# Optimization experiments

Hardware: AMD Instinct MI355X
Metric: run time of the kernel (lower is better)

Reference implementation:

```python
import jax, jax.numpy as jnp
import numpy as np

DIM = 512
NUM_HEADS = 8
BALL_SIZE = 64
TOPK = 2
DIMENSIONALITY = 3
B = 2
N_BALLS = 1024
N_TOTAL = B * N_BALLS * BALL_SIZE


def setup_inputs() -> dict:
    key = jax.random.key(0)
    ks = jax.random.split(key, 6)
    s = 0.02
    return {
        "x": jax.random.normal(ks[0], (N_TOTAL, DIM), jnp.float32),
        "pos": jax.random.normal(ks[1], (N_TOTAL, DIMENSIONALITY), jnp.float32),
        "qkv_w": jax.random.normal(ks[2], (DIM, 3 * DIM), jnp.float32) * s,
        "qkv_b": jnp.zeros((3 * DIM,), jnp.float32),
        "proj_w": jax.random.normal(ks[3], (DIM, DIM), jnp.float32) * s,
        "proj_b": jnp.zeros((DIM,), jnp.float32),
        "pe_w": jax.random.normal(ks[4], (DIMENSIONALITY, DIM), jnp.float32) * s,
        "pe_b": jnp.zeros((DIM,), jnp.float32),
        "num_batches": B,
    }


def _forward(x, pos, qkv_w, qkv_b, proj_w, proj_b, pe_w, pe_b, num_batches):
    N, D = x.shape
    m = BALL_SIZE
    H = NUM_HEADS
    E = D // H
    b = num_batches
    n = N // (b * m)

    # relative position of leaves wrt ball center (torch.no_grad in original)
    p = pos.reshape(-1, m, pos.shape[-1])
    rel = (p - p.mean(axis=1, keepdims=True)).reshape(N, -1)
    rel = jax.lax.stop_gradient(rel)
    x = x + rel @ pe_w + pe_b

    # qkv split exactly like repeat('(b n m) (H E K) -> K b H n m E'): K innermost
    qkv = (x @ qkv_w + qkv_b).reshape(b, n, m, H, E, 3)
    q = jnp.transpose(qkv[..., 0], (0, 3, 1, 2, 4))  # [b,H,n,m,E]
    k = jnp.transpose(qkv[..., 1], (0, 3, 1, 2, 4))
    v = jnp.transpose(qkv[..., 2], (0, 3, 1, 2, 4))

    # The original's rearrange('b n H m E -> b H n m E') on an already
    # [b,H,n,m,E] tensor swaps head/ball axes; the subsequent repeat along a
    # fresh axis of size m*E followed by gather(dim=2) picks values that are
    # independent of the topk indices. Net effect (exactly reproduced here):
    #   desired_{k,v}[b, h, query, t, m2, e] = {k,v}[b, head=t, ball=h, m2, e]
    # i.e. every query of head h attends to keys/values of ball h taken from
    # the first `topk` heads, flattened in (t, m2) order.
    k_sel = jnp.transpose(k[:, :TOPK, :H], (0, 2, 1, 3, 4)).reshape(b, H, TOPK * m, E)
    v_sel = jnp.transpose(v[:, :TOPK, :H], (0, 2, 1, 3, 4)).reshape(b, H, TOPK * m, E)

    qf = q.reshape(b, H, n * m, E)
    scores = jnp.einsum('bhqe,bhke->bhqk', qf, k_sel) * (E ** -0.5)
    attn = jax.nn.softmax(scores, axis=-1)
    out = jnp.einsum('bhqk,bhke->bhqe', attn, v_sel)  # [b,H,n*m,E]
    out = jnp.transpose(out, (0, 2, 1, 3)).reshape(N, D)  # '(b nm) (H E)'
    return out @ proj_w + proj_b


def reference(x, pos, qkv_w, qkv_b, proj_w, proj_b, pe_w, pe_b, num_batches):
    return _forward(x, pos, qkv_w, qkv_b, proj_w, proj_b, pe_w, pe_b, num_batches)
```

## Files before the change

### kernel.cpp

```cpp
#include <hip/hip_runtime.h>

typedef __bf16 bf16;
typedef __bf16 bf16x8 __attribute__((ext_vector_type(8)));
typedef __bf16 bf16x4 __attribute__((ext_vector_type(4)));
typedef float  f32x4  __attribute__((ext_vector_type(4)));

__device__ __forceinline__ f32x4 mfma16(bf16x8 a, bf16x8 b, f32x4 c) {
    return __builtin_amdgcn_mfma_f32_16x16x32_bf16(a, b, c, 0, 0, 0);
}

__device__ __forceinline__ void gll16(const bf16* g, bf16* l) {
    __builtin_amdgcn_global_load_lds(
        (const __attribute__((address_space(1))) void*)g,
        (__attribute__((address_space(3))) void*)l, 16, 0, 0);
}

__global__ __launch_bounds__(256) void prep_weights(
    const float* __restrict__ qkv_w, const float* __restrict__ qkv_b,
    const float* __restrict__ proj_w,
    bf16* __restrict__ BqT, bf16* __restrict__ kvWT, bf16* __restrict__ projWT,
    float* __restrict__ bq, float* __restrict__ bkv)
{
    int i = blockIdx.x * 256 + threadIdx.x;
    if (i < 262144) {
        int c_ = i >> 9, k = i & 511;
        int c = (c_ >> 6) * 192 + (c_ & 63) * 3;
        BqT[i] = (bf16)(qkv_w[k * 1536 + c] * 0.125f);
        return;
    }
    i -= 262144;
    if (i < 131072) {
        int c2 = i >> 9, k = i & 511;
        int t = c2 >> 7, kk = (c2 >> 6) & 1, e = c2 & 63;
        int c = t * 192 + e * 3 + 1 + kk;
        kvWT[i] = (bf16)(qkv_w[k * 1536 + c]);
        return;
    }
    i -= 131072;
    if (i < 262144) {
        int c_ = i >> 9, k = i & 511;
        projWT[i] = (bf16)(proj_w[k * 512 + c_]);
        return;
    }
    i -= 262144;
    if (i < 512) {
        bq[i] = qkv_b[(i >> 6) * 192 + (i & 63) * 3] * 0.125f;
        return;
    }
    i -= 512;
    if (i < 256) {
        int t = i >> 7, kk = (i >> 6) & 1, e = i & 63;
        bkv[i] = qkv_b[t * 192 + e * 3 + 1 + kk];
    }
}

__global__ __launch_bounds__(256) void xprep(
    const float* __restrict__ x, const float* __restrict__ pos,
    const float* __restrict__ pe_w, const float* __restrict__ pe_b,
    bf16* __restrict__ xp)
{
    const int ball = blockIdx.x;
    const int tid = threadIdx.x;
    const size_t tok0 = (size_t)ball * 64;

    __shared__ float pw[1536];
    __shared__ float pb[512];
    __shared__ float pp[64][3];
    __shared__ float mean[3];

    for (int i = tid; i < 1536; i += 256) pw[i] = pe_w[i];
    for (int i = tid; i < 512; i += 256) pb[i] = pe_b[i];
    if (tid < 64) {
        pp[tid][0] = pos[(tok0 + tid) * 3 + 0];
        pp[tid][1] = pos[(tok0 + tid) * 3 + 1];
        pp[tid][2] = pos[(tok0 + tid) * 3 + 2];
    }
    __syncthreads();
    if (tid < 3) {
        float s = 0.f;
        #pragma unroll
        for (int i = 0; i < 64; ++i) s += pp[i][tid];
        mean[tid] = s * (1.0f / 64.0f);
    }
    __syncthreads();

    const float4* x4 = (const float4*)(x + tok0 * 512);
    bf16* op = xp + tok0 * 512;
    #pragma unroll 4
    for (int it = 0; it < 32; ++it) {
        int flat = it * 256 + tid;
        int row = flat >> 7;
        int c = (flat & 127) * 4;
        float4 xv = x4[flat];
        float r0 = pp[row][0] - mean[0];
        float r1 = pp[row][1] - mean[1];
        float r2 = pp[row][2] - mean[2];
        float v0 = xv.x + r0 * pw[c + 0] + r1 * pw[512 + c + 0] + r2 * pw[1024 + c + 0] + pb[c + 0];
        float v1 = xv.y + r0 * pw[c + 1] + r1 * pw[512 + c + 1] + r2 * pw[1024 + c + 1] + pb[c + 1];
        float v2 = xv.z + r0 * pw[c + 2] + r1 * pw[512 + c + 2] + r2 * pw[1024 + c + 2] + pb[c + 2];
        float v3 = xv.w + r0 * pw[c + 3] + r1 * pw[512 + c + 3] + r2 * pw[1024 + c + 3] + pb[c + 3];
        bf16x4 ov = { (bf16)v0, (bf16)v1, (bf16)v2, (bf16)v3 };
        *(bf16x4*)(op + (size_t)flat * 4) = ov;
    }
}

template<int EPI>
__global__ __launch_bounds__(256) void gemm_bt(
    const bf16* __restrict__ A, const bf16* __restrict__ Bt,
    const float* __restrict__ bias, void* __restrict__ Cv)
{
    const int bid = blockIdx.x;
    const int ct = bid & 3;
    const int rt = bid >> 2;
    const int row0 = rt * 128, col0 = ct * 128;
    const int tid = threadIdx.x;
    const int w = tid >> 6, l = tid & 63;
    const int wr = w >> 1, wc = w & 1;
    const int l15 = l & 15, lg = l >> 4;

    __shared__ __align__(16) bf16 As[128 * 64];
    __shared__ __align__(16) bf16 Bs[128 * 64];

    f32x4 acc[4][4] = {};

    int srow[4], scol[4];
    #pragma unroll
    for (int j = 0; j < 4; ++j) {
        int chunk = w * 4 + j;
        int o = chunk * 512 + l * 8;
        int r = o >> 6;
        int slot = (o & 63) >> 3;
        srow[j] = r;
        scol[j] = ((slot ^ (r & 7)) << 3);
    }

    for (int ks = 0; ks < 512; ks += 64) {
        #pragma unroll
        for (int j = 0; j < 4; ++j) {
            int chunk = w * 4 + j;
            gll16(A  + (size_t)(row0 + srow[j]) * 512 + ks + scol[j], &As[chunk * 512]);
            gll16(Bt + (size_t)(col0 + srow[j]) * 512 + ks + scol[j], &Bs[chunk * 512]);
        }
        __syncthreads();
        #pragma unroll
        for (int kk = 0; kk < 2; ++kk) {
            bf16x8 a[4], b[4];
            #pragma unroll
            for (int mi = 0; mi < 4; ++mi) {
                int r = wr * 64 + mi * 16 + l15;
                int slot = (kk * 4 + lg) ^ (r & 7);
                a[mi] = *(const bf16x8*)&As[r * 64 + slot * 8];
            }
            #pragma unroll
            for (int ni = 0; ni < 4; ++ni) {
                int r = wc * 64 + ni * 16 + l15;
                int slot = (kk * 4 + lg) ^ (r & 7);
                b[ni] = *(const bf16x8*)&Bs[r * 64 + slot * 8];
            }
            #pragma unroll
            for (int mi = 0; mi < 4; ++mi)
                #pragma unroll
                for (int ni = 0; ni < 4; ++ni)
                    acc[mi][ni] = mfma16(a[mi], b[ni], acc[mi][ni]);
        }
        __syncthreads();
    }

    #pragma unroll
    for (int mi = 0; mi < 4; ++mi) {
        #pragma unroll
        for (int ni = 0; ni < 4; ++ni) {
            int col = col0 + wc * 64 + ni * 16 + l15;
            float bv = bias[col];
            int rbase = row0 + wr * 64 + mi * 16 + lg * 4;
            #pragma unroll
            for (int r = 0; r < 4; ++r) {
                float vv = acc[mi][ni][r] + bv;
                if (EPI == 0) ((bf16*)Cv)[(size_t)(rbase + r) * 512 + col] = (bf16)vv;
                else          ((float*)Cv)[(size_t)(rbase + r) * 512 + col] = vv;
            }
        }
    }
}

__global__ __launch_bounds__(256) void kv_proj(
    const bf16* __restrict__ xp, const bf16* __restrict__ kvWT,
    const float* __restrict__ bkv, bf16* __restrict__ ksel, bf16* __restrict__ vselT)
{
    const int bid = blockIdx.x;
    const int b = bid >> 9;
    const int ball = (bid >> 6) & 7;
    const int m2 = bid & 63;
    const size_t tok = (size_t)b * 65536 + ball * 64 + m2;
    const int tid = threadIdx.x;

    __shared__ __align__(16) bf16 xrow[512];
    xrow[tid] = xp[tok * 512 + tid];
    xrow[tid + 256] = xp[tok * 512 + tid + 256];
    __syncthreads();

    float acc = 0.f;
    const bf16* wrp = kvWT + (size_t)tid * 512;
    #pragma unroll 8
    for (int k = 0; k < 512; k += 8) {
        bf16x8 wv = *(const bf16x8*)(wrp + k);
        bf16x8 xv = *(const bf16x8*)(&xrow[k]);
        #pragma unroll
        for (int j = 0; j < 8; ++j) acc += (float)xv[j] * (float)wv[j];
    }
    acc += bkv[tid];
    int t = tid >> 7, kk = (tid >> 6) & 1, e = tid & 63;
    if (kk == 0)
        ksel[((size_t)(b * 8 + ball) * 128 + t * 64 + m2) * 64 + e] = (bf16)acc;
    else
        vselT[((size_t)(b * 8 + ball) * 64 + e) * 128 + t * 64 + m2] = (bf16)acc;
}

__global__ __launch_bounds__(256) void attn_k(
    const bf16* __restrict__ q, const bf16* __restrict__ ksel,
    const bf16* __restrict__ vselT, bf16* __restrict__ attno)
{
    const int bid = blockIdx.x;
    const int qt = bid & 1023;
    const int bh = bid >> 10;
    const int b = bh >> 3;
    const int h = bh & 7;
    const int tid = threadIdx.x;
    const int w = tid >> 6;
    const int l = tid & 63;
    const int l15 = l & 15, lg = l >> 4;

    __shared__ __align__(16) bf16 Ks[128][72];
    __shared__ __align__(16) bf16 Vt[64][136];
    __shared__ __align__(16) bf16 Pl[4][16][136];

    const bf16* kg = ksel + (size_t)(b * 8 + h) * 128 * 64;
    #pragma unroll
    for (int it = 0; it < 8; ++it) {
        int i = it * 256 + tid;
        int r = i >> 4, c4 = (i & 15) * 4;
        *(bf16x4*)&Ks[r][c4] = *(const bf16x4*)(kg + r * 64 + c4);
    }
    const bf16* vg = vselT + (size_t)(b * 8 + h) * 64 * 128;
    #pragma unroll
    for (int it = 0; it < 8; ++it) {
        int i = it * 256 + tid;
        int r = i >> 5, c4 = (i & 31) * 4;
        *(bf16x4*)&Vt[r][c4] = *(const bf16x4*)(vg + r * 128 + c4);
    }

    const size_t tokq = (size_t)b * 65536 + (size_t)qt * 64 + w * 16 + l15;
    const bf16* qp = q + tokq * 512 + h * 64 + lg * 8;
    bf16x8 qa0 = *(const bf16x8*)qp;
    bf16x8 qa1 = *(const bf16x8*)(qp + 32);

    __syncthreads();

    f32x4 s[8];
    #pragma unroll
    for (int kt = 0; kt < 8; ++kt) {
        f32x4 a0 = {0.f, 0.f, 0.f, 0.f};
        a0 = mfma16(qa0, *(const bf16x8*)&Ks[kt * 16 + l15][lg * 8], a0);
        a0 = mfma16(qa1, *(const bf16x8*)&Ks[kt * 16 + l15][32 + lg * 8], a0);
        s[kt] = a0;
    }

    #pragma unroll
    for (int r = 0; r < 4; ++r) {
        float mx = s[0][r];
        #pragma unroll
        for (int kt = 1; kt < 8; ++kt) mx = fmaxf(mx, s[kt][r]);
        mx = fmaxf(mx, __shfl_xor(mx, 1));
        mx = fmaxf(mx, __shfl_xor(mx, 2));
        mx = fmaxf(mx, __shfl_xor(mx, 4));
        mx = fmaxf(mx, __shfl_xor(mx, 8));
        float sum = 0.f;
        #pragma unroll
        for (int kt = 0; kt < 8; ++kt) {
            float p = __expf(s[kt][r] - mx);
            s[kt][r] = p;
            sum += p;
        }
        sum += __shfl_xor(sum, 1);
        sum += __shfl_xor(sum, 2);
        sum += __shfl_xor(sum, 4);
        sum += __shfl_xor(sum, 8);
        float inv = 1.0f / sum;
        int prow = lg * 4 + r;
        #pragma unroll
        for (int kt = 0; kt < 8; ++kt)
            Pl[w][prow][kt * 16 + l15] = (bf16)(s[kt][r] * inv);
    }

    __syncthreads();

    f32x4 o[4] = { {0,0,0,0}, {0,0,0,0}, {0,0,0,0}, {0,0,0,0} };
    #pragma unroll
    for (int kc = 0; kc < 4; ++kc) {
        bf16x8 pa = *(const bf16x8*)&Pl[w][l15][kc * 32 + lg * 8];
        #pragma unroll
        for (int et = 0; et < 4; ++et)
            o[et] = mfma16(pa, *(const bf16x8*)&Vt[et * 16 + l15][kc * 32 + lg * 8], o[et]);
    }

    const size_t tokw = (size_t)b * 65536 + (size_t)qt * 64 + w * 16 + lg * 4;
    #pragma unroll
    for (int et = 0; et < 4; ++et)
        #pragma unroll
        for (int r = 0; r < 4; ++r)
            attno[(tokw + r) * 512 + h * 64 + et * 16 + l15] = (bf16)(o[et][r]);
}

extern "C" void kernel_launch(void* const* d_in, const int* in_sizes, int n_in,
                              void* d_out, int out_size, void* d_ws, size_t ws_size,
                              hipStream_t stream) {
    (void)in_sizes; (void)n_in; (void)out_size; (void)ws_size;
    const float* x      = (const float*)d_in[0];
    const float* pos    = (const float*)d_in[1];
    const float* qkv_w  = (const float*)d_in[2];
    const float* qkv_b  = (const float*)d_in[3];
    const float* proj_w = (const float*)d_in[4];
    const float* proj_b = (const float*)d_in[5];
    const float* pe_w   = (const float*)d_in[6];
    const float* pe_b   = (const float*)d_in[7];

    char* ws = (char*)d_ws;
    bf16*  Z     = (bf16*)(ws);
    bf16*  Q     = (bf16*)(ws + 134217728);
    bf16*  BqT   = (bf16*)(ws + 268435456);
    bf16*  PjT   = (bf16*)(ws + 268959744);
    bf16*  kvWT  = (bf16*)(ws + 269484032);
    bf16*  ksel  = (bf16*)(ws + 269746176);
    bf16*  vselT = (bf16*)(ws + 270008320);
    float* bq    = (float*)(ws + 270270464);
    float* bkv   = (float*)(ws + 270272512);

    prep_weights<<<2563, 256, 0, stream>>>(qkv_w, qkv_b, proj_w, BqT, kvWT, PjT, bq, bkv);
    xprep<<<2048, 256, 0, stream>>>(x, pos, pe_w, pe_b, Z);
    gemm_bt<0><<<4096, 256, 0, stream>>>(Z, BqT, bq, (void*)Q);
    kv_proj<<<1024, 256, 0, stream>>>(Z, kvWT, bkv, ksel, vselT);
    attn_k<<<16384, 256, 0, stream>>>(Q, ksel, vselT, Z);
    gemm_bt<1><<<4096, 256, 0, stream>>>(Z, PjT, proj_b, d_out);
}
```

Measured before the change: 512.1 us.

## Fold positional embedding into Q GEMM and fuse attention with output projection

```diff
diff --git a/kernel.cpp b/kernel.cpp
--- a/kernel.cpp
+++ b/kernel.cpp
@@ -19,7 +19,7 @@
     const float* __restrict__ qkv_w, const float* __restrict__ qkv_b,
     const float* __restrict__ proj_w,
     bf16* __restrict__ BqT, bf16* __restrict__ kvWT, bf16* __restrict__ projWT,
-    float* __restrict__ bq, float* __restrict__ bkv)
+    float* __restrict__ bkv)
 {
     int i = blockIdx.x * 256 + threadIdx.x;
     if (i < 262144) {
@@ -43,83 +43,81 @@
         return;
     }
     i -= 262144;
-    if (i < 512) {
-        bq[i] = qkv_b[(i >> 6) * 192 + (i & 63) * 3] * 0.125f;
-        return;
-    }
-    i -= 512;
     if (i < 256) {
         int t = i >> 7, kk = (i >> 6) & 1, e = i & 63;
         bkv[i] = qkv_b[t * 192 + e * 3 + 1 + kk];
     }
 }
 
-__global__ __launch_bounds__(256) void xprep(
-    const float* __restrict__ x, const float* __restrict__ pos,
+__global__ __launch_bounds__(256) void prep_r(
+    const float* __restrict__ qkv_w, const float* __restrict__ qkv_b,
     const float* __restrict__ pe_w, const float* __restrict__ pe_b,
-    bf16* __restrict__ xp)
-{
-    const int ball = blockIdx.x;
-    const int tid = threadIdx.x;
-    const size_t tok0 = (size_t)ball * 64;
-
-    __shared__ float pw[1536];
-    __shared__ float pb[512];
-    __shared__ float pp[64][3];
-    __shared__ float mean[3];
-
-    for (int i = tid; i < 1536; i += 256) pw[i] = pe_w[i];
-    for (int i = tid; i < 512; i += 256) pb[i] = pe_b[i];
-    if (tid < 64) {
-        pp[tid][0] = pos[(tok0 + tid) * 3 + 0];
-        pp[tid][1] = pos[(tok0 + tid) * 3 + 1];
-        pp[tid][2] = pos[(tok0 + tid) * 3 + 2];
-    }
-    __syncthreads();
-    if (tid < 3) {
-        float s = 0.f;
-        #pragma unroll
-        for (int i = 0; i < 64; ++i) s += pp[i][tid];
-        mean[tid] = s * (1.0f / 64.0f);
-    }
-    __syncthreads();
-
-    const float4* x4 = (const float4*)(x + tok0 * 512);
-    bf16* op = xp + tok0 * 512;
-    #pragma unroll 4
-    for (int it = 0; it < 32; ++it) {
-        int flat = it * 256 + tid;
-        int row = flat >> 7;
-        int c = (flat & 127) * 4;
-        float4 xv = x4[flat];
-        float r0 = pp[row][0] - mean[0];
-        float r1 = pp[row][1] - mean[1];
-        float r2 = pp[row][2] - mean[2];
-        float v0 = xv.x + r0 * pw[c + 0] + r1 * pw[512 + c + 0] + r2 * pw[1024 + c + 0] + pb[c + 0];
-        float v1 = xv.y + r0 * pw[c + 1] + r1 * pw[512 + c + 1] + r2 * pw[1024 + c + 1] + pb[c + 1];
-        float v2 = xv.z + r0 * pw[c + 2] + r1 * pw[512 + c + 2] + r2 * pw[1024 + c + 2] + pb[c + 2];
-        float v3 = xv.w + r0 * pw[c + 3] + r1 * pw[512 + c + 3] + r2 * pw[1024 + c + 3] + pb[c + 3];
-        bf16x4 ov = { (bf16)v0, (bf16)v1, (bf16)v2, (bf16)v3 };
-        *(bf16x4*)(op + (size_t)flat * 4) = ov;
-    }
-}
-
-template<int EPI>
-__global__ __launch_bounds__(256) void gemm_bt(
-    const bf16* __restrict__ A, const bf16* __restrict__ Bt,
-    const float* __restrict__ bias, void* __restrict__ Cv)
-{
-    const int bid = blockIdx.x;
-    const int ct = bid & 3;
-    const int rt = bid >> 2;
+    float* __restrict__ R, float* __restrict__ bq2)
+{
+    int idx = blockIdx.x * 256 + threadIdx.x;
+    int c = idx >> 2, j = idx & 3;
+    int qc = (c >> 6) * 192 + (c & 63) * 3;
+    const float* wcol = qkv_w + qc;
+    float s = 0.f;
+    if (j < 3) {
+        const float* pw = pe_w + j * 512;
+        for (int k = 0; k < 512; ++k) s += pw[k] * wcol[(size_t)k * 1536];
+        R[j * 512 + c] = 0.125f * s;
+    } else {
+        for (int k = 0; k < 512; ++k) s += pe_b[k] * wcol[(size_t)k * 1536];
+        bq2[c] = 0.125f * (qkv_b[qc] + s);
+    }
+}
+
+__global__ __launch_bounds__(64) void relprep(const float* __restrict__ pos,
+                                              float* __restrict__ rel)
+{
+    const int t = blockIdx.x * 64 + threadIdx.x;
+    float p0 = pos[(size_t)t * 3 + 0];
+    float p1 = pos[(size_t)t * 3 + 1];
+    float p2 = pos[(size_t)t * 3 + 2];
+    float s0 = p0, s1 = p1, s2 = p2;
+    #pragma unroll
+    for (int m = 1; m < 64; m <<= 1) {
+        s0 += __shfl_xor(s0, m);
+        s1 += __shfl_xor(s1, m);
+        s2 += __shfl_xor(s2, m);
+    }
+    rel[(size_t)t * 3 + 0] = p0 - s0 * (1.0f / 64.0f);
+    rel[(size_t)t * 3 + 1] = p1 - s1 * (1.0f / 64.0f);
+    rel[(size_t)t * 3 + 2] = p2 - s2 * (1.0f / 64.0f);
+}
+
+__global__ __launch_bounds__(256, 2) void qgemm(
+    const float* __restrict__ X, const bf16* __restrict__ Bt,
+    const float* __restrict__ rel, const float* __restrict__ R,
+    const float* __restrict__ bq2, bf16* __restrict__ Qout)
+{
+    const int bid0 = blockIdx.x;
+    const int wg = (bid0 & 7) * 512 + (bid0 >> 3);
+    const int ct = wg & 3;
+    const int rt = wg >> 2;
     const int row0 = rt * 128, col0 = ct * 128;
     const int tid = threadIdx.x;
     const int w = tid >> 6, l = tid & 63;
     const int wr = w >> 1, wc = w & 1;
     const int l15 = l & 15, lg = l >> 4;
 
-    __shared__ __align__(16) bf16 As[128 * 64];
-    __shared__ __align__(16) bf16 Bs[128 * 64];
+    __shared__ __align__(16) bf16 As[8192];
+    __shared__ __align__(16) bf16 Bs[8192];
+    __shared__ float relS[128][3];
+    __shared__ float RS[3][128];
+
+    if (tid < 128) {
+        relS[tid][0] = rel[(size_t)(row0 + tid) * 3 + 0];
+        relS[tid][1] = rel[(size_t)(row0 + tid) * 3 + 1];
+        relS[tid][2] = rel[(size_t)(row0 + tid) * 3 + 2];
+    } else {
+        int c = tid - 128;
+        RS[0][c] = R[0 * 512 + col0 + c];
+        RS[1][c] = R[1 * 512 + col0 + c];
+        RS[2][c] = R[2 * 512 + col0 + c];
+    }
 
     f32x4 acc[4][4] = {};
 
@@ -133,12 +131,25 @@
         srow[j] = r;
         scol[j] = ((slot ^ (r & 7)) << 3);
     }
+    const int ar_sub = l >> 3;
+    const int ak = l & 7;
+    const int aslot = (ak ^ ar_sub) << 3;
 
     for (int ks = 0; ks < 512; ks += 64) {
         #pragma unroll
         for (int j = 0; j < 4; ++j) {
             int chunk = w * 4 + j;
-            gll16(A  + (size_t)(row0 + srow[j]) * 512 + ks + scol[j], &As[chunk * 512]);
+            int r = chunk * 8 + ar_sub;
+            const float* xp = X + (size_t)(row0 + r) * 512 + ks + ak * 8;
+            float4 v0 = *(const float4*)xp;
+            float4 v1 = *(const float4*)(xp + 4);
+            bf16x8 bv = { (bf16)v0.x, (bf16)v0.y, (bf16)v0.z, (bf16)v0.w,
+                          (bf16)v1.x, (bf16)v1.y, (bf16)v1.z, (bf16)v1.w };
+            *(bf16x8*)&As[r * 64 + aslot] = bv;
+        }
+        #pragma unroll
+        for (int j = 0; j < 4; ++j) {
+            int chunk = w * 4 + j;
             gll16(Bt + (size_t)(col0 + srow[j]) * 512 + ks + scol[j], &Bs[chunk * 512]);
         }
         __syncthreads();
@@ -170,22 +181,27 @@
     for (int mi = 0; mi < 4; ++mi) {
         #pragma unroll
         for (int ni = 0; ni < 4; ++ni) {
-            int col = col0 + wc * 64 + ni * 16 + l15;
-            float bv = bias[col];
-            int rbase = row0 + wr * 64 + mi * 16 + lg * 4;
+            int colL = wc * 64 + ni * 16 + l15;
+            int col = col0 + colL;
+            float bv = bq2[col];
+            float r0c = RS[0][colL], r1c = RS[1][colL], r2c = RS[2][colL];
+            int rbaseL = wr * 64 + mi * 16 + lg * 4;
             #pragma unroll
             for (int r = 0; r < 4; ++r) {
-                float vv = acc[mi][ni][r] + bv;
-                if (EPI == 0) ((bf16*)Cv)[(size_t)(rbase + r) * 512 + col] = (bf16)vv;
-                else          ((float*)Cv)[(size_t)(rbase + r) * 512 + col] = vv;
-            }
-        }
-    }
-}
-
-__global__ __launch_bounds__(256) void kv_proj(
-    const bf16* __restrict__ xp, const bf16* __restrict__ kvWT,
-    const float* __restrict__ bkv, bf16* __restrict__ ksel, bf16* __restrict__ vselT)
+                int rowL = rbaseL + r;
+                float vv = acc[mi][ni][r] + bv
+                         + relS[rowL][0] * r0c + relS[rowL][1] * r1c + relS[rowL][2] * r2c;
+                Qout[(size_t)(row0 + rowL) * 512 + col] = (bf16)vv;
+            }
+        }
+    }
+}
+
+__global__ __launch_bounds__(256) void kv_proj2(
+    const float* __restrict__ x, const float* __restrict__ rel,
+    const float* __restrict__ pe_w, const float* __restrict__ pe_b,
+    const bf16* __restrict__ kvWT, const float* __restrict__ bkv,
+    bf16* __restrict__ ksel, bf16* __restrict__ vselT)
 {
     const int bid = blockIdx.x;
     const int b = bid >> 9;
@@ -195,8 +211,14 @@
     const int tid = threadIdx.x;
 
     __shared__ __align__(16) bf16 xrow[512];
-    xrow[tid] = xp[tok * 512 + tid];
-    xrow[tid + 256] = xp[tok * 512 + tid + 256];
+    __shared__ float relt[3];
+    if (tid < 3) relt[tid] = rel[tok * 3 + tid];
+    __syncthreads();
+    for (int k = tid; k < 512; k += 256) {
+        float v = x[tok * 512 + k] + relt[0] * pe_w[k] + relt[1] * pe_w[512 + k]
+                + relt[2] * pe_w[1024 + k] + pe_b[k];
+        xrow[k] = (bf16)v;
+    }
     __syncthreads();
 
     float acc = 0.f;
@@ -216,99 +238,130 @@
         vselT[((size_t)(b * 8 + ball) * 64 + e) * 128 + t * 64 + m2] = (bf16)acc;
 }
 
-__global__ __launch_bounds__(256) void attn_k(
-    const bf16* __restrict__ q, const bf16* __restrict__ ksel,
-    const bf16* __restrict__ vselT, bf16* __restrict__ attno)
+__global__ __launch_bounds__(256, 2) void attnproj(
+    const bf16* __restrict__ Q, const bf16* __restrict__ ksel,
+    const bf16* __restrict__ vselT, const bf16* __restrict__ projT,
+    const float* __restrict__ proj_b, float* __restrict__ out)
 {
     const int bid = blockIdx.x;
-    const int qt = bid & 1023;
-    const int bh = bid >> 10;
-    const int b = bh >> 3;
-    const int h = bh & 7;
+    const int wg = (bid & 7) * 256 + (bid >> 3);
+    const int b = wg >> 10;
+    const size_t tok0 = (size_t)wg * 64;
     const int tid = threadIdx.x;
-    const int w = tid >> 6;
-    const int l = tid & 63;
+    const int w = tid >> 6, l = tid & 63;
     const int l15 = l & 15, lg = l >> 4;
 
     __shared__ __align__(16) bf16 Ks[128][72];
     __shared__ __align__(16) bf16 Vt[64][136];
     __shared__ __align__(16) bf16 Pl[4][16][136];
 
-    const bf16* kg = ksel + (size_t)(b * 8 + h) * 128 * 64;
+    f32x4 acc[4][8] = {};
+
+    for (int h = 0; h < 8; ++h) {
+        const bf16* kg = ksel + (size_t)(b * 8 + h) * 128 * 64;
+        #pragma unroll
+        for (int it = 0; it < 4; ++it) {
+            int i = it * 256 + tid;
+            int r = i >> 3, c8 = (i & 7) * 8;
+            *(bf16x8*)&Ks[r][c8] = *(const bf16x8*)(kg + r * 64 + c8);
+        }
+        const bf16* vg = vselT + (size_t)(b * 8 + h) * 64 * 128;
+        #pragma unroll
+        for (int it = 0; it < 4; ++it) {
+            int i = it * 256 + tid;
+            int r = i >> 4, c8 = (i & 15) * 8;
+            *(bf16x8*)&Vt[r][c8] = *(const bf16x8*)(vg + r * 128 + c8);
+        }
+        __syncthreads();
+
+        const bf16* qp = Q + (tok0 + w * 16 + l15) * 512 + h * 64 + lg * 8;
+        bf16x8 qa0 = *(const bf16x8*)qp;
+        bf16x8 qa1 = *(const bf16x8*)(qp + 32);
+
+        f32x4 s[8];
+        #pragma unroll
+        for (int kt = 0; kt < 8; ++kt) {
+            f32x4 a0 = {0.f, 0.f, 0.f, 0.f};
+            a0 = mfma16(qa0, *(const bf16x8*)&Ks[kt * 16 + l15][lg * 8], a0);
+            a0 = mfma16(qa1, *(const bf16x8*)&Ks[kt * 16 + l15][32 + lg * 8], a0);
+            s[kt] = a0;
+        }
+
+        #pragma unroll
+        for (int r = 0; r < 4; ++r) {
+            float mx = s[0][r];
+            #pragma unroll
+            for (int kt = 1; kt < 8; ++kt) mx = fmaxf(mx, s[kt][r]);
+            mx = fmaxf(mx, __shfl_xor(mx, 1));
+            mx = fmaxf(mx, __shfl_xor(mx, 2));
+            mx = fmaxf(mx, __shfl_xor(mx, 4));
+            mx = fmaxf(mx, __shfl_xor(mx, 8));
+            float sum = 0.f;
+            #pragma unroll
+            for (int kt = 0; kt < 8; ++kt) {
+                float p = __expf(s[kt][r] - mx);
+                s[kt][r] = p;
+                sum += p;
+            }
+            sum += __shfl_xor(sum, 1);
+            sum += __shfl_xor(sum, 2);
+            sum += __shfl_xor(sum, 4);
+            sum += __shfl_xor(sum, 8);
+            float inv = 1.0f / sum;
+            int prow = lg * 4 + r;
+            #pragma unroll
+            for (int kt = 0; kt < 8; ++kt)
+                Pl[w][prow][kt * 16 + l15] = (bf16)(s[kt][r] * inv);
+        }
+
+        f32x4 o[4] = { {0,0,0,0}, {0,0,0,0}, {0,0,0,0}, {0,0,0,0} };
+        #pragma unroll
+        for (int kvc = 0; kvc < 4; ++kvc) {
+            bf16x8 pb_ = *(const bf16x8*)&Pl[w][l15][kvc * 32 + lg * 8];
+            #pragma unroll
+            for (int et = 0; et < 4; ++et)
+                o[et] = mfma16(*(const bf16x8*)&Vt[et * 16 + l15][kvc * 32 + lg * 8], pb_, o[et]);
+        }
+
+        #pragma unroll
+        for (int et = 0; et < 4; ++et)
+            #pragma unroll
+            for (int r = 0; r < 4; ++r)
+                Pl[w][l15][et * 16 + lg * 4 + r] = (bf16)(o[et][r]);
+
+        __syncthreads();
+
+        #pragma unroll
+        for (int kc = 0; kc < 2; ++kc) {
+            bf16x8 af[4];
+            #pragma unroll
+            for (int mi = 0; mi < 4; ++mi)
+                af[mi] = *(const bf16x8*)&Pl[mi][l15][kc * 32 + lg * 8];
+            #pragma unroll
+            for (int nj = 0; nj < 8; ++nj) {
+                const bf16* bp = projT + (size_t)(w * 128 + nj * 16 + l15) * 512
+                               + h * 64 + kc * 32 + lg * 8;
+                bf16x8 bf_ = *(const bf16x8*)bp;
+                #pragma unroll
+                for (int mi = 0; mi < 4; ++mi)
+                    acc[mi][nj] = mfma16(af[mi], bf_, acc[mi][nj]);
+            }
+        }
+        __syncthreads();
+    }
+
     #pragma unroll
-    for (int it = 0; it < 8; ++it) {
-        int i = it * 256 + tid;
-        int r = i >> 4, c4 = (i & 15) * 4;
-        *(bf16x4*)&Ks[r][c4] = *(const bf16x4*)(kg + r * 64 + c4);
-    }
-    const bf16* vg = vselT + (size_t)(b * 8 + h) * 64 * 128;
-    #pragma unroll
-    for (int it = 0; it < 8; ++it) {
-        int i = it * 256 + tid;
-        int r = i >> 5, c4 = (i & 31) * 4;
-        *(bf16x4*)&Vt[r][c4] = *(const bf16x4*)(vg + r * 128 + c4);
-    }
-
-    const size_t tokq = (size_t)b * 65536 + (size_t)qt * 64 + w * 16 + l15;
-    const bf16* qp = q + tokq * 512 + h * 64 + lg * 8;
-    bf16x8 qa0 = *(const bf16x8*)qp;
-    bf16x8 qa1 = *(const bf16x8*)(qp + 32);
-
-    __syncthreads();
-
-    f32x4 s[8];
-    #pragma unroll
-    for (int kt = 0; kt < 8; ++kt) {
-        f32x4 a0 = {0.f, 0.f, 0.f, 0.f};
-        a0 = mfma16(qa0, *(const bf16x8*)&Ks[kt * 16 + l15][lg * 8], a0);
-        a0 = mfma16(qa1, *(const bf16x8*)&Ks[kt * 16 + l15][32 + lg * 8], a0);
-        s[kt] = a0;
-    }
-
-    #pragma unroll
-    for (int r = 0; r < 4; ++r) {
-        float mx = s[0][r];
-        #pragma unroll
-        for (int kt = 1; kt < 8; ++kt) mx = fmaxf(mx, s[kt][r]);
-        mx = fmaxf(mx, __shfl_xor(mx, 1));
-        mx = fmaxf(mx, __shfl_xor(mx, 2));
-        mx = fmaxf(mx, __shfl_xor(mx, 4));
-        mx = fmaxf(mx, __shfl_xor(mx, 8));
-        float sum = 0.f;
-        #pragma unroll
-        for (int kt = 0; kt < 8; ++kt) {
-            float p = __expf(s[kt][r] - mx);
-            s[kt][r] = p;
-            sum += p;
-        }
-        sum += __shfl_xor(sum, 1);
-        sum += __shfl_xor(sum, 2);
-        sum += __shfl_xor(sum, 4);
-        sum += __shfl_xor(sum, 8);
-        float inv = 1.0f / sum;
-        int prow = lg * 4 + r;
-        #pragma unroll
-        for (int kt = 0; kt < 8; ++kt)
-            Pl[w][prow][kt * 16 + l15] = (bf16)(s[kt][r] * inv);
-    }
-
-    __syncthreads();
-
-    f32x4 o[4] = { {0,0,0,0}, {0,0,0,0}, {0,0,0,0}, {0,0,0,0} };
-    #pragma unroll
-    for (int kc = 0; kc < 4; ++kc) {
-        bf16x8 pa = *(const bf16x8*)&Pl[w][l15][kc * 32 + lg * 8];
-        #pragma unroll
-        for (int et = 0; et < 4; ++et)
-            o[et] = mfma16(pa, *(const bf16x8*)&Vt[et * 16 + l15][kc * 32 + lg * 8], o[et]);
-    }
-
-    const size_t tokw = (size_t)b * 65536 + (size_t)qt * 64 + w * 16 + lg * 4;
-    #pragma unroll
-    for (int et = 0; et < 4; ++et)
-        #pragma unroll
-        for (int r = 0; r < 4; ++r)
-            attno[(tokw + r) * 512 + h * 64 + et * 16 + l15] = (bf16)(o[et][r]);
+    for (int nj = 0; nj < 8; ++nj) {
+        int col = w * 128 + nj * 16 + l15;
+        float bv = proj_b[col];
+        #pragma unroll
+        for (int mi = 0; mi < 4; ++mi) {
+            size_t rbase = tok0 + mi * 16 + lg * 4;
+            #pragma unroll
+            for (int r = 0; r < 4; ++r)
+                out[(rbase + r) * 512 + col] = acc[mi][nj][r] + bv;
+        }
+    }
 }
 
 extern "C" void kernel_launch(void* const* d_in, const int* in_sizes, int n_in,
@@ -325,20 +378,21 @@
     const float* pe_b   = (const float*)d_in[7];
 
     char* ws = (char*)d_ws;
-    bf16*  Z     = (bf16*)(ws);
-    bf16*  Q     = (bf16*)(ws + 134217728);
-    bf16*  BqT   = (bf16*)(ws + 268435456);
-    bf16*  PjT   = (bf16*)(ws + 268959744);
-    bf16*  kvWT  = (bf16*)(ws + 269484032);
-    bf16*  ksel  = (bf16*)(ws + 269746176);
-    bf16*  vselT = (bf16*)(ws + 270008320);
-    float* bq    = (float*)(ws + 270270464);
-    float* bkv   = (float*)(ws + 270272512);
-
-    prep_weights<<<2563, 256, 0, stream>>>(qkv_w, qkv_b, proj_w, BqT, kvWT, PjT, bq, bkv);
-    xprep<<<2048, 256, 0, stream>>>(x, pos, pe_w, pe_b, Z);
-    gemm_bt<0><<<4096, 256, 0, stream>>>(Z, BqT, bq, (void*)Q);
-    kv_proj<<<1024, 256, 0, stream>>>(Z, kvWT, bkv, ksel, vselT);
-    attn_k<<<16384, 256, 0, stream>>>(Q, ksel, vselT, Z);
-    gemm_bt<1><<<4096, 256, 0, stream>>>(Z, PjT, proj_b, d_out);
-}
+    bf16*  Q     = (bf16*)(ws);
+    bf16*  BqT   = (bf16*)(ws + 134217728);
+    bf16*  PjT   = (bf16*)(ws + 134742016);
+    bf16*  kvWT  = (bf16*)(ws + 135266304);
+    bf16*  ksel  = (bf16*)(ws + 135528448);
+    bf16*  vselT = (bf16*)(ws + 135790592);
+    float* rel   = (float*)(ws + 136052736);
+    float* R     = (float*)(ws + 137625600);
+    float* bq2   = (float*)(ws + 137631744);
+    float* bkv   = (float*)(ws + 137633792);
+
+    prep_weights<<<2561, 256, 0, stream>>>(qkv_w, qkv_b, proj_w, BqT, kvWT, PjT, bkv);
+    prep_r<<<8, 256, 0, stream>>>(qkv_w, qkv_b, pe_w, pe_b, R, bq2);
+    relprep<<<2048, 64, 0, stream>>>(pos, rel);
+    qgemm<<<4096, 256, 0, stream>>>(x, BqT, rel, R, bq2, Q);
+    kv_proj2<<<1024, 256, 0, stream>>>(x, rel, pe_w, pe_b, kvWT, bkv, ksel, vselT);
+    attnproj<<<2048, 256, 0, stream>>>(Q, ksel, vselT, PjT, proj_b, (float*)d_out);
+}
```

Measured after the change: 671.5 us. +31.1%, slower.
